# Optimization experiments

Measured on AMD Instinct MI355X. Metric: run time of the kernel, lower is better.

The kernel has to match this reference:

```python
import jax, jax.numpy as jnp
import numpy as np

B, C, D, H, W = 4, 256, 16, 16, 16
REDUCTION = 8
CR = C // REDUCTION  # q/k channel dim = 32


def setup_inputs() -> dict:
    key = jax.random.key(0)
    k1, k2, k3, k4, k5, k6 = jax.random.split(key, 6)
    x = jax.random.normal(k1, (B, C, D, H, W), dtype=jnp.float32)
    # 1x1x1 conv weights are just [out_ch, in_ch] matrices
    Wq = jax.random.normal(k2, (CR, C), dtype=jnp.float32) * (1.0 / np.sqrt(C))
    Wk = jax.random.normal(k3, (CR, C), dtype=jnp.float32) * (1.0 / np.sqrt(C))
    Wv = jax.random.normal(k4, (C, C), dtype=jnp.float32) * (1.0 / np.sqrt(C))
    Wo = jax.random.normal(k5, (C, C), dtype=jnp.float32) * (1.0 / np.sqrt(C))
    gamma = jnp.zeros((1,), dtype=jnp.float32) + 0.5  # nonzero so output depends on attention
    return {"x": x, "Wq": Wq, "Wk": Wk, "Wv": Wv, "Wo": Wo, "gamma": gamma}


def reference(x, Wq, Wk, Wv, Wo, gamma):
    b, c, d, h, w = x.shape
    n = d * h * w
    scale = Wq.shape[0] ** -0.5  # (channels // reduction) ** -0.5
    xf = x.reshape(b, c, n)                      # [B, C, N]
    q = jnp.einsum('oc,bcn->bon', Wq, xf)        # [B, CR, N]
    k = jnp.einsum('oc,bcn->bon', Wk, xf)        # [B, CR, N]
    v = jnp.einsum('oc,bcn->bon', Wv, xf)        # [B, C, N]
    attn = jax.nn.softmax(jnp.einsum('bcn,bcm->bnm', q, k) * scale, axis=-1)  # [B, N, N]
    out = jnp.einsum('bcm,bnm->bcn', v, attn)    # v @ attn^T -> [B, C, N]
    out = jnp.einsum('oc,bcn->bon', Wo, out)     # output 1x1x1 conv
    out = out.reshape(b, c, d, h, w)
    return gamma[0] * out + x
```

## Files before the change

### kernel.cpp

```cpp
#include <hip/hip_runtime.h>
#include <hip/hip_bf16.h>

#define BATCH 4
#define CH 256
#define CRD 32
#define NN 4096

typedef __bf16 bf16x8 __attribute__((ext_vector_type(8)));
typedef float floatx4 __attribute__((ext_vector_type(4)));
typedef float floatx16 __attribute__((ext_vector_type(16)));
typedef unsigned short ushort4v __attribute__((ext_vector_type(4)));
typedef unsigned short ushort8v __attribute__((ext_vector_type(8)));
typedef unsigned int uint2v __attribute__((ext_vector_type(2)));
typedef unsigned int uint4v __attribute__((ext_vector_type(4)));

static __device__ __forceinline__ unsigned short f2bf(float f) {
    __bf16 h = (__bf16)f;
    return __builtin_bit_cast(unsigned short, h);
}
static __device__ __forceinline__ float bf2f(unsigned short h) {
    return __uint_as_float((unsigned int)h << 16);
}


__global__ __launch_bounds__(256) void wconv_kernel(
    const float* __restrict__ Wq, const float* __restrict__ Wk,
    const float* __restrict__ Wv, const float* __restrict__ Wo,
    unsigned short* __restrict__ What, unsigned short* __restrict__ WobF)
{
    const int o = blockIdx.x;
    const int t = threadIdx.x;
    float scale = 1.0f;
    const float* src;
    if (o < 32)      { src = Wq + o * 256;
                       scale = 0.17677669529663687f * 1.4426950408889634f; }
    else if (o < 64) { src = Wk + (o - 32) * 256; }
    else             { src = Wv + (o - 64) * 256; }
    const int mb = o >> 5;
    const size_t idx = ((size_t)(mb * 16 + (t >> 4)) * 64
                        + (o & 31) + 32 * ((t >> 3) & 1)) * 8 + (t & 7);
    What[idx] = f2bf(src[t] * scale);
    if (o < 256) {
        const size_t i2 = ((size_t)((o >> 5) * 16 + (t >> 4)) * 64
                           + (o & 31) + 32 * ((t >> 3) & 1)) * 8 + (t & 7);
        WobF[i2] = f2bf(Wo[o * 256 + t]);
    }
}

static __device__ __forceinline__ uint4v hmerge(
    const ushort4v& xp, const ushort4v& yp, int h)
{
    uint2v xd = __builtin_bit_cast(uint2v, xp);
    uint2v yd = __builtin_bit_cast(uint2v, yp);
    unsigned int px0 = (unsigned int)__shfl_xor((int)xd[0], 32);
    unsigned int px1 = (unsigned int)__shfl_xor((int)xd[1], 32);
    unsigned int py0 = (unsigned int)__shfl_xor((int)yd[0], 32);
    unsigned int py1 = (unsigned int)__shfl_xor((int)yd[1], 32);
    uint4v st;
    st[0] = h ? py0 : xd[0];
    st[1] = h ? py1 : xd[1];
    st[2] = h ? yd[0] : px0;
    st[3] = h ? yd[1] : px1;
    return st;
}

__global__ __launch_bounds__(256, 2) void qkv_kernel(
    const float* __restrict__ x, const unsigned short* __restrict__ What,
    unsigned short* __restrict__ qh, unsigned short* __restrict__ kh,
    unsigned short* __restrict__ vh)
{
    __shared__ __align__(16) unsigned short xf[16 * 512];

    const int t = threadIdx.x;
    const int w = t >> 6;
    const int l = t & 63;
    const int l31 = l & 31;
    const int h = l >> 5;
    const int nt = blockIdx.x, b = blockIdx.y;
    const int n0 = nt * 32;

    {
        const float* xb = x + (size_t)(b * CH) * NN + n0;
        const int n = t & 31;
        const int cq = t >> 5;
        #pragma unroll
        for (int p = 0; p < 8; ++p) {
            int c = p * 32 + cq * 4;
            float v0 = xb[(size_t)(c + 0) * NN + n];
            float v1 = xb[(size_t)(c + 1) * NN + n];
            float v2 = xb[(size_t)(c + 2) * NN + n];
            float v3 = xb[(size_t)(c + 3) * NN + n];
            ushort4v u4;
            u4[0] = f2bf(v0); u4[1] = f2bf(v1); u4[2] = f2bf(v2); u4[3] = f2bf(v3);
            int addr = ((2 * p + (cq >> 2)) * 64 + n + 32 * ((cq >> 1) & 1)) * 8
                       + 4 * (cq & 1);
            *(ushort4v*)&xf[addr] = u4;
        }
    }
    __syncthreads();

    const int mb0 = w, mb1 = w + 4, mb2 = w + 8;
    floatx16 acc0, acc1, acc2;
    #pragma unroll
    for (int i = 0; i < 16; ++i) { acc0[i] = 0.f; acc1[i] = 0.f; acc2[i] = 0.f; }

    for (int kblk = 0; kblk < 16; ++kblk) {
        bf16x8 bf = *(const bf16x8*)&xf[kblk * 512 + l * 8];
        bf16x8 a0 = *(const bf16x8*)(What + ((size_t)(mb0 * 16 + kblk) * 64 + l) * 8);
        bf16x8 a1 = *(const bf16x8*)(What + ((size_t)(mb1 * 16 + kblk) * 64 + l) * 8);
        acc0 = __builtin_amdgcn_mfma_f32_32x32x16_bf16(a0, bf, acc0, 0, 0, 0);
        acc1 = __builtin_amdgcn_mfma_f32_32x32x16_bf16(a1, bf, acc1, 0, 0, 0);
        if (w < 2) {
            bf16x8 a2 = *(const bf16x8*)(What + ((size_t)(mb2 * 16 + kblk) * 64 + l) * 8);
            acc2 = __builtin_amdgcn_mfma_f32_32x32x16_bf16(a2, bf, acc2, 0, 0, 0);
        }
    }

    auto store_qk = [&](unsigned short* dst, const floatx16& a) {
        size_t base = (size_t)(b * 128 + nt) * 1024;
        #pragma unroll
        for (int sb = 0; sb < 2; ++sb) {
            ushort4v xp, yp;
            #pragma unroll
            for (int i = 0; i < 4; ++i) {
                xp[i] = f2bf(a[8 * sb + i]);
                yp[i] = f2bf(a[8 * sb + 4 + i]);
            }
            uint4v st = hmerge(xp, yp, h);
            *(uint4v*)(dst + base + (size_t)sb * 512 + (size_t)l * 8) = st;
        }
    };

    if (w == 0)      store_qk(qh, acc0);
    else if (w == 1) store_qk(kh, acc0);

    __syncthreads();

    auto store_v_lds = [&](int cblk, const floatx16& a) {
        const int chunk = cblk * 2 + (l31 >> 4);
        const int hib = (l31 >> 3) & 1;
        #pragma unroll
        for (int r = 0; r < 16; ++r) {
            int rowo = (r & 3) + 8 * (r >> 2) + 4 * h;
            int unit = chunk * 64 + hib * 32 + rowo;
            int pu = unit ^ ((unit >> 5) & 7);
            xf[pu * 8 + (l31 & 7)] = f2bf(a[r]);
        }
    };

    if (w >= 2) store_v_lds(w - 2, acc0);
    store_v_lds(w + 2, acc1);
    if (w < 2) store_v_lds(w + 6, acc2);

    __syncthreads();

    #pragma unroll
    for (int p = 0; p < 4; ++p) {
        int Lu = p * 256 + t;
        int pu = Lu ^ ((Lu >> 5) & 7);
        uint4v d = *(const uint4v*)&xf[pu * 8];
        int chunk = Lu >> 6;
        int cblk = chunk >> 1, sub = chunk & 1;
        size_t dst = (((size_t)b * 8 + cblk) * 256 + nt * 2 + sub) * 512
                     + (size_t)(Lu & 63) * 8;
        *(uint4v*)(vh + dst) = d;
    }
}

#define SM_M0 12.0f

__global__ __launch_bounds__(512, 4) void attn_kernel(
    const unsigned short* __restrict__ qh, const unsigned short* __restrict__ kh,
    const unsigned short* __restrict__ vh, unsigned short* __restrict__ Opart,
    float* __restrict__ ml)
{
    __shared__ unsigned short p_lds[2 * 16 * 64 * 8];
    __shared__ float psum_s[8][32];

    const int t = threadIdx.x;
    const int w = t >> 6;
    const int l = t & 63;
    const int l31 = l & 31;
    const int h = l >> 5;
    const int wk = w & 3;
    const int hq = w >> 2;

    const int lin = blockIdx.x + ((int)blockIdx.y << 6) + ((int)blockIdx.z << 8);
    const int slot = lin >> 3;
    const int combo = ((lin & 7) << 1) | (slot >> 6);
    const int gp = slot & 63;
    const int ks = combo & 3;
    const int b  = combo >> 2;
    const int g0 = 2 * gp, g1 = 2 * gp + 1;

    const unsigned short* qB = qh + (size_t)(b * 128 + (hq ? g1 : g0)) * 1024;
    const unsigned short* kB = kh + (size_t)b * 128 * 1024;
    const unsigned short* vB = vh + (size_t)b * 8 * 256 * 512;

    bf16x8 qf0 = *(const bf16x8*)(qB + l * 8);
    bf16x8 qf1 = *(const bf16x8*)(qB + 512 + l * 8);

    bf16x8 kf0 = *(const bf16x8*)(kB + (size_t)(ks * 32 + wk) * 1024 + l * 8);
    bf16x8 kf1 = *(const bf16x8*)(kB + (size_t)(ks * 32 + wk) * 1024 + 512 + l * 8);

    float l_loc = 0.f;
    floatx16 acc_a, acc_b;
    #pragma unroll
    for (int i = 0; i < 16; ++i) { acc_a[i] = 0.f; acc_b[i] = 0.f; }

    for (int it = 0; it < 8; ++it) {
        const int pbase = (it & 1) << 13;

        floatx16 sacc;
        #pragma unroll
        for (int i = 0; i < 16; ++i) sacc[i] = 0.f;
        __builtin_amdgcn_s_setprio(1);
        sacc = __builtin_amdgcn_mfma_f32_32x32x16_bf16(kf0, qf0, sacc, 0, 0, 0);
        sacc = __builtin_amdgcn_mfma_f32_32x32x16_bf16(kf1, qf1, sacc, 0, 0, 0);
        __builtin_amdgcn_s_setprio(0);

        float pv[16];
        #pragma unroll
        for (int r = 0; r < 16; ++r) pv[r] = __builtin_exp2f(sacc[r] - SM_M0);
        float s0 = (pv[0] + pv[1]) + (pv[2] + pv[3]);
        float s1 = (pv[4] + pv[5]) + (pv[6] + pv[7]);
        float s2 = (pv[8] + pv[9]) + (pv[10] + pv[11]);
        float s3 = (pv[12] + pv[13]) + (pv[14] + pv[15]);
        l_loc += (s0 + s1) + (s2 + s3);
        #pragma unroll
        for (int rg = 0; rg < 4; ++rg) {
            ushort4v pk;
            #pragma unroll
            for (int i = 0; i < 4; ++i) pk[i] = f2bf(pv[rg * 4 + i]);
            int idx = pbase
                    + ((hq * 8 + 2 * wk + (rg >> 1)) * 64
                       + l31 + 32 * (rg & 1)) * 8 + 4 * h;
            *(ushort4v*)&p_lds[idx] = pk;
        }
        if (it < 7) {
            const unsigned short* kn = kB + (size_t)(ks * 32 + (it + 1) * 4 + wk) * 1024;
            kf0 = *(const bf16x8*)(kn + l * 8);
            kf1 = *(const bf16x8*)(kn + 512 + l * 8);
        }
        const unsigned short* v0b = vB + ((size_t)w * 256 + (ks * 8 + it) * 8) * 512;
        bf16x8 va0 = *(const bf16x8*)(v0b + 0 * 512 + l * 8);
        bf16x8 va1 = *(const bf16x8*)(v0b + 1 * 512 + l * 8);
        bf16x8 va2 = *(const bf16x8*)(v0b + 2 * 512 + l * 8);
        bf16x8 va3 = *(const bf16x8*)(v0b + 3 * 512 + l * 8);
        bf16x8 va4 = *(const bf16x8*)(v0b + 4 * 512 + l * 8);
        bf16x8 va5 = *(const bf16x8*)(v0b + 5 * 512 + l * 8);
        bf16x8 va6 = *(const bf16x8*)(v0b + 6 * 512 + l * 8);
        bf16x8 va7 = *(const bf16x8*)(v0b + 7 * 512 + l * 8);

        __syncthreads();

        bf16x8 pa = *(const bf16x8*)&p_lds[pbase + l * 8];
        bf16x8 pb = *(const bf16x8*)&p_lds[pbase + 4096 + l * 8];
        #pragma unroll
        for (int s = 0; s < 8; ++s) {
            bf16x8 vcur = (s == 0) ? va0 : (s == 1) ? va1 : (s == 2) ? va2
                        : (s == 3) ? va3 : (s == 4) ? va4 : (s == 5) ? va5
                        : (s == 6) ? va6 : va7;
            bf16x8 pa_n, pb_n;
            if (s < 7) {
                pa_n = *(const bf16x8*)&p_lds[pbase + ((s + 1) * 64 + l) * 8];
                pb_n = *(const bf16x8*)&p_lds[pbase + 4096 + ((s + 1) * 64 + l) * 8];
            }
            __builtin_amdgcn_s_setprio(1);
            acc_a = __builtin_amdgcn_mfma_f32_32x32x16_bf16(vcur, pa, acc_a, 0, 0, 0);
            acc_b = __builtin_amdgcn_mfma_f32_32x32x16_bf16(vcur, pb, acc_b, 0, 0, 0);
            __builtin_amdgcn_s_setprio(0);
            pa = pa_n; pb = pb_n;
        }
    }

    float lt = l_loc + __shfl_xor(l_loc, 32);
    if (h == 0) psum_s[w][l31] = lt;
    __syncthreads();

    if (w == 0 && h == 0) {
        float l_run = (psum_s[0][l31] + psum_s[1][l31])
                    + (psum_s[2][l31] + psum_s[3][l31]);
        size_t mb = ((size_t)(b * 128 + g0) * 4 + ks) * 64;
        ml[mb + l31] = SM_M0;
        ml[mb + 32 + l31] = l_run;
    }
    if (w == 4 && h == 0) {
        float l_run = (psum_s[4][l31] + psum_s[5][l31])
                    + (psum_s[6][l31] + psum_s[7][l31]);
        size_t mb = ((size_t)(b * 128 + g1) * 4 + ks) * 64;
        ml[mb + l31] = SM_M0;
        ml[mb + 32 + l31] = l_run;
    }

    unsigned short* opa = Opart + ((size_t)((b * 128 + g0) * 4 + ks)) * 8192;
    unsigned short* opb = Opart + ((size_t)((b * 128 + g1) * 4 + ks)) * 8192;
    #pragma unroll
    for (int ct = 0; ct < 2; ++ct) {
        const floatx16& a = ct ? acc_b : acc_a;
        unsigned short* op = ct ? opb : opa;
        #pragma unroll
        for (int sb = 0; sb < 2; ++sb) {
            ushort4v xp, yp;
            #pragma unroll
            for (int i = 0; i < 4; ++i) {
                xp[i] = f2bf(a[8 * sb + i]);
                yp[i] = f2bf(a[8 * sb + 4 + i]);
            }
            uint4v st = hmerge(xp, yp, h);
            int sP = 2 * w + sb;
            *(uint4v*)(op + ((size_t)sP * 64 + l) * 8) = st;
        }
    }
}

__global__ __launch_bounds__(256, 2) void out_kernel(
    const unsigned short* __restrict__ Opart, const float* __restrict__ ml,
    const unsigned short* __restrict__ WobF, const float* __restrict__ x,
    const float* __restrict__ gamma, float* __restrict__ out)
{
    const int t = threadIdx.x;
    const int w = t >> 6;
    const int l = t & 63;
    const int l31 = l & 31;
    const int h = l >> 5;
    const int qt = blockIdx.x, b = blockIdx.y;

    const size_t slot = (size_t)(b * 128 + qt) * 4;
    float m0 = ml[(slot + 0) * 64 + l31], l0 = ml[(slot + 0) * 64 + 32 + l31];
    float m1 = ml[(slot + 1) * 64 + l31], l1 = ml[(slot + 1) * 64 + 32 + l31];
    float m2 = ml[(slot + 2) * 64 + l31], l2 = ml[(slot + 2) * 64 + 32 + l31];
    float m3 = ml[(slot + 3) * 64 + l31], l3 = ml[(slot + 3) * 64 + 32 + l31];
    float M = fmaxf(fmaxf(m0, m1), fmaxf(m2, m3));
    float e0 = __builtin_exp2f(m0 - M), e1 = __builtin_exp2f(m1 - M);
    float e2 = __builtin_exp2f(m2 - M), e3 = __builtin_exp2f(m3 - M);
    float Lc = l0 * e0 + l1 * e1 + l2 * e2 + l3 * e3;
    float rL = 1.0f / Lc;
    float w0 = e0 * rL, w1 = e1 * rL, w2 = e2 * rL, w3 = e3 * rL;

    const unsigned short* o0 = Opart + (slot + 0) * 8192;
    const unsigned short* o1 = Opart + (slot + 1) * 8192;
    const unsigned short* o2 = Opart + (slot + 2) * 8192;
    const unsigned short* o3 = Opart + (slot + 3) * 8192;

    floatx16 acc[2];
    #pragma unroll
    for (int m = 0; m < 2; ++m)
        #pragma unroll
        for (int i = 0; i < 16; ++i) acc[m][i] = 0.f;

    for (int s = 0; s < 16; ++s) {
        ushort8v f0 = *(const ushort8v*)(o0 + (s * 64 + l) * 8);
        ushort8v f1 = *(const ushort8v*)(o1 + (s * 64 + l) * 8);
        ushort8v f2 = *(const ushort8v*)(o2 + (s * 64 + l) * 8);
        ushort8v f3 = *(const ushort8v*)(o3 + (s * 64 + l) * 8);
        ushort8v cmb;
        #pragma unroll
        for (int j = 0; j < 8; ++j)
            cmb[j] = f2bf(w0 * bf2f(f0[j]) + w1 * bf2f(f1[j])
                        + w2 * bf2f(f2[j]) + w3 * bf2f(f3[j]));
        bf16x8 bfr = *(bf16x8*)&cmb;
        #pragma unroll
        for (int m = 0; m < 2; ++m) {
            int mt = 2 * w + m;
            bf16x8 af = *(const bf16x8*)(WobF + ((size_t)(mt * 16 + s) * 64 + l) * 8);
            acc[m] = __builtin_amdgcn_mfma_f32_32x32x16_bf16(af, bfr, acc[m], 0, 0, 0);
        }
    }

    const float gm = gamma[0];
    #pragma unroll
    for (int m = 0; m < 2; ++m)
        #pragma unroll
        for (int r = 0; r < 16; ++r) {
            int o = (2 * w + m) * 32 + (r & 3) + 8 * (r >> 2) + 4 * h;
            int n = qt * 32 + l31;
            size_t oi = ((size_t)(b * 256 + o)) * NN + n;
            out[oi] = gm * acc[m][r] + x[oi];
        }
}

extern "C" void kernel_launch(void* const* d_in, const int* in_sizes, int n_in,
                              void* d_out, int out_size, void* d_ws, size_t ws_size,
                              hipStream_t stream)
{
    const float* x     = (const float*)d_in[0];
    const float* Wq    = (const float*)d_in[1];
    const float* Wk    = (const float*)d_in[2];
    const float* Wv    = (const float*)d_in[3];
    const float* Wo    = (const float*)d_in[4];
    const float* gamma = (const float*)d_in[5];
    float* out = (float*)d_out;

    char* wsb = (char*)d_ws;
    unsigned short* qh    = (unsigned short*)(wsb);
    unsigned short* kh    = (unsigned short*)(wsb + (1u << 20));
    unsigned short* vh    = (unsigned short*)(wsb + (2u << 20));
    unsigned short* What  = (unsigned short*)(wsb + (10u << 20));
    unsigned short* WobF  = (unsigned short*)(wsb + (10u << 20) + (256u << 10));
    unsigned short* Opart = (unsigned short*)(wsb + (11u << 20));
    float*          ml    = (float*)         (wsb + (45u << 20));

    wconv_kernel<<<320, 256, 0, stream>>>(Wq, Wk, Wv, Wo, What, WobF);

    dim3 g1(128, BATCH);
    qkv_kernel<<<g1, 256, 0, stream>>>(x, What, qh, kh, vh);

    dim3 g2(64, 4, BATCH);
    attn_kernel<<<g2, 512, 0, stream>>>(qh, kh, vh, Opart, ml);

    dim3 g3(128, BATCH);
    out_kernel<<<g3, 256, 0, stream>>>(Opart, ml, WobF, x, gamma, out);
}
```

Measured before the change: 149.5 us.

## Halve attention key-split count and combine partials via per-split MFMA accumulation

The attention kernel now splits the key dimension into 2 chunks instead of 4, so each block loops 16 iterations and the grid is halved. Because the softmax max is a fixed constant, only the row sums are stored. The output kernel no longer rescales and mixes partial outputs elementwise. Instead it runs separate MFMAs against each partial and divides by the summed normaliser at the end. This cuts partial-output traffic and combine work, at the cost of fewer attention blocks (512) and less parallelism per wave.

After: 150.9 us. About the same (+1.0%).

```diff
diff --git a/kernel.cpp b/kernel.cpp
--- a/kernel.cpp
+++ b/kernel.cpp
@@ -185,12 +185,11 @@
     const int wk = w & 3;
     const int hq = w >> 2;
 
-    const int lin = blockIdx.x + ((int)blockIdx.y << 6) + ((int)blockIdx.z << 8);
-    const int slot = lin >> 3;
-    const int combo = ((lin & 7) << 1) | (slot >> 6);
-    const int gp = slot & 63;
-    const int ks = combo & 3;
-    const int b  = combo >> 2;
+    const int lin = blockIdx.x + ((int)blockIdx.y << 6) + ((int)blockIdx.z << 7);
+    const int combo = lin & 7;
+    const int gp = lin >> 3;
+    const int ks = combo & 1;
+    const int b  = combo >> 1;
     const int g0 = 2 * gp, g1 = 2 * gp + 1;
 
     const unsigned short* qB = qh + (size_t)(b * 128 + (hq ? g1 : g0)) * 1024;
@@ -200,15 +199,15 @@
     bf16x8 qf0 = *(const bf16x8*)(qB + l * 8);
     bf16x8 qf1 = *(const bf16x8*)(qB + 512 + l * 8);
 
-    bf16x8 kf0 = *(const bf16x8*)(kB + (size_t)(ks * 32 + wk) * 1024 + l * 8);
-    bf16x8 kf1 = *(const bf16x8*)(kB + (size_t)(ks * 32 + wk) * 1024 + 512 + l * 8);
+    bf16x8 kf0 = *(const bf16x8*)(kB + (size_t)(ks * 64 + wk) * 1024 + l * 8);
+    bf16x8 kf1 = *(const bf16x8*)(kB + (size_t)(ks * 64 + wk) * 1024 + 512 + l * 8);
 
     float l_loc = 0.f;
     floatx16 acc_a, acc_b;
     #pragma unroll
     for (int i = 0; i < 16; ++i) { acc_a[i] = 0.f; acc_b[i] = 0.f; }
 
-    for (int it = 0; it < 8; ++it) {
+    for (int it = 0; it < 16; ++it) {
         const int pbase = (it & 1) << 13;
 
         floatx16 sacc;
@@ -237,12 +236,12 @@
                        + l31 + 32 * (rg & 1)) * 8 + 4 * h;
             *(ushort4v*)&p_lds[idx] = pk;
         }
-        if (it < 7) {
-            const unsigned short* kn = kB + (size_t)(ks * 32 + (it + 1) * 4 + wk) * 1024;
+        if (it < 15) {
+            const unsigned short* kn = kB + (size_t)(ks * 64 + (it + 1) * 4 + wk) * 1024;
             kf0 = *(const bf16x8*)(kn + l * 8);
             kf1 = *(const bf16x8*)(kn + 512 + l * 8);
         }
-        const unsigned short* v0b = vB + ((size_t)w * 256 + (ks * 8 + it) * 8) * 512;
+        const unsigned short* v0b = vB + ((size_t)w * 256 + (ks * 16 + it) * 8) * 512;
         bf16x8 va0 = *(const bf16x8*)(v0b + 0 * 512 + l * 8);
         bf16x8 va1 = *(const bf16x8*)(v0b + 1 * 512 + l * 8);
         bf16x8 va2 = *(const bf16x8*)(v0b + 2 * 512 + l * 8);
@@ -281,20 +280,16 @@
     if (w == 0 && h == 0) {
         float l_run = (psum_s[0][l31] + psum_s[1][l31])
                     + (psum_s[2][l31] + psum_s[3][l31]);
-        size_t mb = ((size_t)(b * 128 + g0) * 4 + ks) * 64;
-        ml[mb + l31] = SM_M0;
-        ml[mb + 32 + l31] = l_run;
+        ml[((size_t)(b * 128 + g0) * 2 + ks) * 32 + l31] = l_run;
     }
     if (w == 4 && h == 0) {
         float l_run = (psum_s[4][l31] + psum_s[5][l31])
                     + (psum_s[6][l31] + psum_s[7][l31]);
-        size_t mb = ((size_t)(b * 128 + g1) * 4 + ks) * 64;
-        ml[mb + l31] = SM_M0;
-        ml[mb + 32 + l31] = l_run;
-    }
-
-    unsigned short* opa = Opart + ((size_t)((b * 128 + g0) * 4 + ks)) * 8192;
-    unsigned short* opb = Opart + ((size_t)((b * 128 + g1) * 4 + ks)) * 8192;
+        ml[((size_t)(b * 128 + g1) * 2 + ks) * 32 + l31] = l_run;
+    }
+
+    unsigned short* opa = Opart + ((size_t)((b * 128 + g0) * 2 + ks)) * 8192;
+    unsigned short* opb = Opart + ((size_t)((b * 128 + g1) * 2 + ks)) * 8192;
     #pragma unroll
     for (int ct = 0; ct < 2; ++ct) {
         const floatx16& a = ct ? acc_b : acc_a;
@@ -326,45 +321,30 @@
     const int h = l >> 5;
     const int qt = blockIdx.x, b = blockIdx.y;
 
-    const size_t slot = (size_t)(b * 128 + qt) * 4;
-    float m0 = ml[(slot + 0) * 64 + l31], l0 = ml[(slot + 0) * 64 + 32 + l31];
-    float m1 = ml[(slot + 1) * 64 + l31], l1 = ml[(slot + 1) * 64 + 32 + l31];
-    float m2 = ml[(slot + 2) * 64 + l31], l2 = ml[(slot + 2) * 64 + 32 + l31];
-    float m3 = ml[(slot + 3) * 64 + l31], l3 = ml[(slot + 3) * 64 + 32 + l31];
-    float M = fmaxf(fmaxf(m0, m1), fmaxf(m2, m3));
-    float e0 = __builtin_exp2f(m0 - M), e1 = __builtin_exp2f(m1 - M);
-    float e2 = __builtin_exp2f(m2 - M), e3 = __builtin_exp2f(m3 - M);
-    float Lc = l0 * e0 + l1 * e1 + l2 * e2 + l3 * e3;
-    float rL = 1.0f / Lc;
-    float w0 = e0 * rL, w1 = e1 * rL, w2 = e2 * rL, w3 = e3 * rL;
-
-    const unsigned short* o0 = Opart + (slot + 0) * 8192;
-    const unsigned short* o1 = Opart + (slot + 1) * 8192;
-    const unsigned short* o2 = Opart + (slot + 2) * 8192;
-    const unsigned short* o3 = Opart + (slot + 3) * 8192;
-
-    floatx16 acc[2];
+    const size_t slot2 = (size_t)(b * 128 + qt) * 2;
+    float l0 = ml[(slot2 + 0) * 32 + l31];
+    float l1 = ml[(slot2 + 1) * 32 + l31];
+    float rL = 1.0f / (l0 + l1);
+
+    const unsigned short* o0 = Opart + (slot2 + 0) * 8192;
+    const unsigned short* o1 = Opart + (slot2 + 1) * 8192;
+
+    floatx16 a0[2], a1[2];
     #pragma unroll
     for (int m = 0; m < 2; ++m)
         #pragma unroll
-        for (int i = 0; i < 16; ++i) acc[m][i] = 0.f;
-
+        for (int i = 0; i < 16; ++i) { a0[m][i] = 0.f; a1[m][i] = 0.f; }
+
+    #pragma unroll 2
     for (int s = 0; s < 16; ++s) {
-        ushort8v f0 = *(const ushort8v*)(o0 + (s * 64 + l) * 8);
-        ushort8v f1 = *(const ushort8v*)(o1 + (s * 64 + l) * 8);
-        ushort8v f2 = *(const ushort8v*)(o2 + (s * 64 + l) * 8);
-        ushort8v f3 = *(const ushort8v*)(o3 + (s * 64 + l) * 8);
-        ushort8v cmb;
-        #pragma unroll
-        for (int j = 0; j < 8; ++j)
-            cmb[j] = f2bf(w0 * bf2f(f0[j]) + w1 * bf2f(f1[j])
-                        + w2 * bf2f(f2[j]) + w3 * bf2f(f3[j]));
-        bf16x8 bfr = *(bf16x8*)&cmb;
+        bf16x8 f0 = *(const bf16x8*)(o0 + (s * 64 + l) * 8);
+        bf16x8 f1 = *(const bf16x8*)(o1 + (s * 64 + l) * 8);
         #pragma unroll
         for (int m = 0; m < 2; ++m) {
             int mt = 2 * w + m;
             bf16x8 af = *(const bf16x8*)(WobF + ((size_t)(mt * 16 + s) * 64 + l) * 8);
-            acc[m] = __builtin_amdgcn_mfma_f32_32x32x16_bf16(af, bfr, acc[m], 0, 0, 0);
+            a0[m] = __builtin_amdgcn_mfma_f32_32x32x16_bf16(af, f0, a0[m], 0, 0, 0);
+            a1[m] = __builtin_amdgcn_mfma_f32_32x32x16_bf16(af, f1, a1[m], 0, 0, 0);
         }
     }
 
@@ -373,10 +353,11 @@
     for (int m = 0; m < 2; ++m)
         #pragma unroll
         for (int r = 0; r < 16; ++r) {
+            float v = (a0[m][r] + a1[m][r]) * rL;
             int o = (2 * w + m) * 32 + (r & 3) + 8 * (r >> 2) + 4 * h;
             int n = qt * 32 + l31;
             size_t oi = ((size_t)(b * 256 + o)) * NN + n;
-            out[oi] = gm * acc[m][r] + x[oi];
+            out[oi] = gm * v + x[oi];
         }
 }
 
@@ -406,7 +387,7 @@
     dim3 g1(128, BATCH);
     qkv_kernel<<<g1, 256, 0, stream>>>(x, What, qh, kh, vh);
 
-    dim3 g2(64, 4, BATCH);
+    dim3 g2(64, 2, BATCH);
     attn_kernel<<<g2, 512, 0, stream>>>(qh, kh, vh, Opart, ml);
 
     dim3 g3(128, BATCH);
```
